# Kernel optimization log

Measured on AMD Instinct MI355X. Metric: run time of the kernel, lower is better.

The kernel has to match this reference:

```python
import jax, jax.numpy as jnp
import numpy as np

PS = 8; STRIDE = 1; NVALS = 31
DELTA = 0.05; ETA = 0.01; TAU = 0.1
B = 2; CIN = 32; H = 64; W = 64
HP = (H - PS) // STRIDE + 1
WP = (W - PS) // STRIDE + 1
TWO_PI = 2.0 * np.pi

# patch-local coordinate grid (torch.meshgrid 'ij': y varies along rows)
_lin = np.linspace(-1.0, 1.0, PS).astype(np.float32)
YG = jnp.asarray(np.tile(_lin[:, None], (1, PS)))[None, :, :, None, None]  # [1,ps,ps,1,1]
XG = jnp.asarray(np.tile(_lin[None, :], (PS, 1)))[None, :, :, None, None]

ANGLE_RANGE = jnp.asarray(np.linspace(0.0, TWO_PI, NVALS + 1, dtype=np.float32)[:NVALS])
XY_RANGE = jnp.asarray(np.linspace(-3.0, 3.0, NVALS, dtype=np.float32))

# unfold/fold index maps: pixel (hp*stride + px, wp*stride + py)
RI = jnp.arange(PS)[:, None] + STRIDE * jnp.arange(HP)[None, :]  # [ps,hp]
CI = jnp.arange(PS)[:, None] + STRIDE * jnp.arange(WP)[None, :]  # [ps,wp]
R4 = RI[:, None, :, None]  # [ps,1,hp,1]
C4 = CI[None, :, None, :]  # [1,ps,1,wp]


def conv1x1(x, w):
    return jnp.einsum('bchw,oc->bohw', x, w)


def bn(x, gamma, beta, eps=1e-5):
    # BatchNorm2d in training mode: batch statistics, biased variance
    m = x.mean(axis=(0, 2, 3), keepdims=True)
    v = x.var(axis=(0, 2, 3), keepdims=True)
    return gamma[None, :, None, None] * (x - m) * jax.lax.rsqrt(v + eps) + beta[None, :, None, None]


def silu(x):
    return x * jax.nn.sigmoid(x)


def params_to_distances(params):
    # params: [n,5,hp,wp] -> dists [n,2,ps,ps,hp,wp]
    x0 = params[:, 3][:, None, None]  # [n,1,1,hp,wp]
    y0 = params[:, 4][:, None, None]
    ang = jnp.sort(jnp.mod(params[:, :3], TWO_PI), axis=1)
    a1 = ang[:, 0][:, None, None]
    a2 = ang[:, 1][:, None, None]
    a3 = ang[:, 2][:, None, None]
    a4 = 0.5 * (a1 + a3) + jnp.where(jnp.mod(0.5 * (a1 - a3), TWO_PI) >= np.pi, np.pi, 0.0)

    def g(dt):
        return (dt / np.pi - 1.0) ** 35

    def line(a):
        return -jnp.sin(a) * (XG - x0) + jnp.cos(a) * (YG - y0)

    d42 = jnp.mod(a2 - a4, TWO_PI)
    sgn42 = jnp.where(d42 < np.pi, 1.0, -1.0)
    dist42 = sgn42 * jnp.minimum(sgn42 * line(a4), -sgn42 * line(a2)) + g(d42) * TAU
    d13 = jnp.mod(a3 - a1, TWO_PI)
    sgn13 = jnp.where(d13 < np.pi, 1.0, -1.0)
    dist13 = sgn13 * jnp.minimum(sgn13 * line(a1), -sgn13 * line(a3)) + g(d13) * TAU
    return jnp.stack([dist13, dist42], axis=1)


def wedges_of(dists):
    hd = 0.5 * (1.0 + (2.0 / np.pi) * jnp.arctan(dists / ETA))
    h0, h1 = hd[:, 0], hd[:, 1]
    return jnp.stack([1.0 - h0, h0 * (1.0 - h1), h0 * h1], axis=1)  # [n,3,ps,ps,hp,wp]


def dcp(params, imgp):
    # params [n,5,hp,wp], imgp [c,ps,ps,hp,wp]
    dists = params_to_distances(params)
    w = wedges_of(dists)
    wsum = w.sum(axis=(2, 3))  # [n,3,hp,wp]
    cnum = jnp.einsum('cxyHW,nkxyHW->nckHW', imgp, w)
    colors = cnum / (wsum[:, None] + 1e-10)  # [n,c,3,hp,wp]
    patches = jnp.einsum('nkxyHW,nckHW->ncxyHW', w, colors)
    return dists, colors, patches


def boundaries_of(dists):
    d1, d2 = dists[:, 0:1], dists[:, 1:2]
    mad = jnp.where(d1 < 0.0, -d1,
                    jnp.where(d2 < 0.0, jnp.minimum(d1, -d2), jnp.minimum(d1, d2)))
    return 1.0 / (1.0 + (mad / DELTA) ** 2)


def fold(patches):
    # [B,C,ps,ps,hp,wp] -> [B,C,H,W] (sum over overlapping patches)
    Bn, C = patches.shape[:2]
    return jnp.zeros((Bn, C, H, W), patches.dtype).at[:, :, R4, C4].add(patches)


def forward(x, reduce_w, reduce_gamma, reduce_beta, fb_w, fb_gamma, fb_beta, fi_w, fi_gamma, fi_beta):
    xr = silu(bn(conv1x1(x, reduce_w), reduce_gamma, reduce_beta))  # [B,3,H,W]
    imgp = xr[:, :, R4, C4]  # unfold -> [B,3,ps,ps,hp,wp]
    num_patches = jnp.zeros((H, W), xr.dtype).at[R4, C4].add(
        jnp.ones((PS, PS, HP, WP), xr.dtype))

    params = jnp.zeros((x.shape[0], 5, HP, WP), xr.dtype)

    def make_step(i, prange):
        def step(p_b, imgp_b):
            pq = jnp.repeat(p_b[None], NVALS, axis=0)  # [n,5,hp,wp]
            pq = pq.at[:, i].add(prange[:, None, None])
            _, _, patches = dcp(pq, imgp_b)
            loss = ((imgp_b[None] - patches) ** 2).mean(axis=(2, 3)).sum(axis=1)  # [n,hp,wp]
            best = jnp.argmin(loss, axis=0)
            vals = jnp.take_along_axis(pq[:, i], best[None], axis=0)[0]
            return p_b.at[i].set(vals)
        return step

    for i in range(5):  # coordinate descent over 3 angles then x0, y0
        prange = ANGLE_RANGE if i < 3 else XY_RANGE
        params = jax.vmap(make_step(i, prange))(params, imgp)

    def finalize(p_b, imgp_b):
        dists, _, patches = dcp(p_b[None], imgp_b)
        return patches[0], boundaries_of(dists)[0]

    patches_all, lb_all = jax.vmap(finalize)(params, imgp)
    smoothed = fold(patches_all) / num_patches[None, None]  # [B,3,H,W]
    gb = fold(lb_all) / num_patches[None, None]             # [B,1,H,W]
    gb3 = jnp.broadcast_to(gb, (gb.shape[0], 3, H, W))
    boundaries = silu(bn(conv1x1(gb3, fb_w), fb_gamma, fb_beta))
    image = silu(bn(conv1x1(smoothed, fi_w), fi_gamma, fi_beta))
    return boundaries, image


def setup_inputs() -> dict:
    key = jax.random.key(0)
    ks = jax.random.split(key, 4)
    return {
        'x': jax.random.normal(ks[0], (B, CIN, H, W), jnp.float32),
        'reduce_w': jax.random.normal(ks[1], (3, CIN), jnp.float32) * 0.1,
        'reduce_gamma': jnp.ones((3,), jnp.float32),
        'reduce_beta': jnp.zeros((3,), jnp.float32),
        'fb_w': jax.random.normal(ks[2], (1, 3), jnp.float32) * 0.3,
        'fb_gamma': jnp.ones((1,), jnp.float32),
        'fb_beta': jnp.zeros((1,), jnp.float32),
        'fi_w': jax.random.normal(ks[3], (1, 3), jnp.float32) * 0.3,
        'fi_gamma': jnp.ones((1,), jnp.float32),
        'fi_beta': jnp.zeros((1,), jnp.float32),
    }


def reference(x, reduce_w, reduce_gamma, reduce_beta, fb_w, fb_gamma, fb_beta, fi_w, fi_gamma, fi_beta):
    return forward(x, reduce_w, reduce_gamma, reduce_beta, fb_w, fb_gamma, fb_beta, fi_w, fi_gamma, fi_beta)
```

## Files before the change

### kernel.cpp

```cpp
#include <hip/hip_runtime.h>
#include <math.h>

#define B_    2
#define CIN_  32
#define H_    64
#define W_    64
#define HP_   57
#define WP_   57
#define NP_   (B_*HP_*WP_)
#define NVALS_ 31

#define XR_OFF   0
#define FP_OFF   24576
#define FG_OFF   49152
#define ST_OFF   57344
#define TMPB_OFF 57360
#define TMPI_OFF 65552
#define WS_TOTAL 73744

static __device__ __forceinline__ float mod2pi(float x) {
    const float TP = (float)(2.0 * M_PI);
    float m = fmodf(x, TP);
    return (m < 0.0f) ? (m + TP) : m;
}
static __device__ __forceinline__ float pow35f(float t) {
    float t2 = t * t, t4 = t2 * t2, t8 = t4 * t4, t16 = t8 * t8, t32 = t16 * t16;
    return t32 * t2 * t;
}
static __device__ __forceinline__ float siluf(float x) {
    return x / (1.0f + expf(-x));
}
static __device__ __forceinline__ float wave_sum(float v) {
#pragma unroll
    for (int m = 1; m < 64; m <<= 1) v += __shfl_xor(v, m);
    return v;
}
static __device__ __forceinline__ float lin_of(int k) {
    return (float)(-1.0 + (double)k * (2.0 / 7.0));
}

struct Geo {
    float X1, Y1, X3, Y3;
    float X4, Y4, X2, Y2;
    float sgn13, sgn42, g13, g42, x0, y0;
};

static __device__ void setup_geo(float p0, float p1, float p2, float p3, float p4,
                                 Geo& G) {
    const float PIF = (float)M_PI;
    float m0 = mod2pi(p0), m1 = mod2pi(p1), m2 = mod2pi(p2);
    float lo = fminf(m0, m1), hi = fmaxf(m0, m1);
    float a1 = fminf(lo, m2);
    float a3 = fmaxf(hi, m2);
    float a2 = fmaxf(fminf(hi, m2), lo);
    float hm = mod2pi(0.5f * (a1 - a3));
    float a4 = 0.5f * (a1 + a3) + ((hm >= PIF) ? PIF : 0.0f);
    float d42 = mod2pi(a2 - a4);
    G.sgn42 = (d42 < PIF) ? 1.0f : -1.0f;
    G.g42 = pow35f(d42 / PIF - 1.0f) * 0.1f;
    float d13 = mod2pi(a3 - a1);
    G.sgn13 = (d13 < PIF) ? 1.0f : -1.0f;
    G.g13 = pow35f(d13 / PIF - 1.0f) * 0.1f;
    float s1 = sinf(a1), c1 = cosf(a1);
    float s2 = sinf(a2), c2 = cosf(a2);
    float s3 = sinf(a3), c3 = cosf(a3);
    float s4 = sinf(a4), c4 = cosf(a4);
    G.X1 = -G.sgn13 * s1;  G.Y1 =  G.sgn13 * c1;
    G.X3 =  G.sgn13 * s3;  G.Y3 = -G.sgn13 * c3;
    G.X4 = -G.sgn42 * s4;  G.Y4 =  G.sgn42 * c4;
    G.X2 =  G.sgn42 * s2;  G.Y2 = -G.sgn42 * c2;
    G.x0 = p3; G.y0 = p4;
}

static __device__ __forceinline__ void dists_at(const Geo& G, float xg, float yg,
                                                float& d13, float& d42) {
    float dx = xg - G.x0, dy = yg - G.y0;
    float u1 = G.X1 * dx + G.Y1 * dy;
    float u3 = G.X3 * dx + G.Y3 * dy;
    float u4 = G.X4 * dx + G.Y4 * dy;
    float u2 = G.X2 * dx + G.Y2 * dy;
    d13 = G.sgn13 * fminf(u1, u3) + G.g13;
    d42 = G.sgn42 * fminf(u4, u2) + G.g42;
}

static __device__ __forceinline__ void wedge_of(float d13, float d42,
                                                float& w0, float& w1, float& w2) {
    const float C2OPI = (float)(2.0 / M_PI);
    float hd0 = 0.5f * (1.0f + C2OPI * atanf(d13 * 100.0f));
    float hd1 = 0.5f * (1.0f + C2OPI * atanf(d42 * 100.0f));
    w0 = 1.0f - hd0;
    w1 = hd0 * (1.0f - hd1);
    w2 = hd0 * hd1;
}

__global__ __launch_bounds__(128) void head_in_conv(const float* __restrict__ x,
                                                    const float* __restrict__ rw,
                                                    float* __restrict__ xr,
                                                    float* __restrict__ st) {
    const int e = blockIdx.x * 128 + threadIdx.x;
    const int b = e >> 12, rem = e & 4095;
    const float* xp = x + (size_t)b * CIN_ * 4096 + rem;
    float a0 = 0.0f, a1 = 0.0f, a2 = 0.0f;
#pragma unroll
    for (int c = 0; c < CIN_; ++c) {
        float xv = xp[c * 4096];
        a0 += rw[c] * xv;
        a1 += rw[32 + c] * xv;
        a2 += rw[64 + c] * xv;
    }
    xr[(b * 3 + 0) * 4096 + rem] = a0;
    xr[(b * 3 + 1) * 4096 + rem] = a1;
    xr[(b * 3 + 2) * 4096 + rem] = a2;
    float s0 = wave_sum(a0), q0 = wave_sum(a0 * a0);
    float s1 = wave_sum(a1), q1 = wave_sum(a1 * a1);
    float s2 = wave_sum(a2), q2 = wave_sum(a2 * a2);
    if ((threadIdx.x & 63) == 0) {
        atomicAdd(&st[0], s0); atomicAdd(&st[1], s1); atomicAdd(&st[2], s2);
        atomicAdd(&st[3], q0); atomicAdd(&st[4], q1); atomicAdd(&st[5], q2);
    }
}

__global__ __launch_bounds__(256) void mega_kernel(const float* __restrict__ xr,
                                                   const float* __restrict__ gamma,
                                                   const float* __restrict__ beta,
                                                   const float* __restrict__ st,
                                                   float* __restrict__ foldP,
                                                   float* __restrict__ foldG) {
    __shared__ float s_img[4][192];
    __shared__ float s_lin[8];
    const int t = threadIdx.x;
    if (t < 8) s_lin[t] = lin_of(t);
    const int lg = t >> 6, lane = t & 63;
    const int patch = blockIdx.x * 4 + lg;
    const bool active = (patch < NP_);
    int b = 0, hp = 0, wp = 0;
    if (active) {
        b = patch / (HP_ * WP_);
        int pi = patch - b * (HP_ * WP_);
        hp = pi / WP_; wp = pi - hp * WP_;
        const int pr = lane >> 3, pc = lane & 7;
        const int goff = ((hp + pr) << 6) + (wp + pc);
#pragma unroll
        for (int c = 0; c < 3; ++c) {
            float mean = st[c] / 8192.0f;
            float var  = st[3 + c] / 8192.0f - mean * mean;
            float sc = gamma[c] / sqrtf(var + 1e-5f);
            float sh = beta[c] - mean * sc;
            float v  = xr[((b * 3 + c) << 12) + goff];
            s_img[lg][64 * c + lane] = siluf(v * sc + sh);
        }
    }
    __syncthreads();
    if (!active) return;

    const int cand = lane >> 1;
    const int half = lane & 1;
    const float* img = s_img[lg] + half * 32;
    const int yoff = half << 2;

    float p0 = 0.0f, p1 = 0.0f, p2 = 0.0f, p3 = 0.0f, p4 = 0.0f;

#pragma unroll 1
    for (int step = 0; step < 5; ++step) {
        const float base = (step == 0) ? p0 : (step == 1) ? p1 :
                           (step == 2) ? p2 : (step == 3) ? p3 : p4;
        const int ci = (cand < NVALS_) ? cand : (NVALS_ - 1);
        float add;
        if (step < 3) add = (float)((double)ci * (6.283185307179586476925286766559 / 31.0));
        else          add = (float)(-3.0 + (double)ci * 0.2);
        const float pv = base + add;
        Geo G;
        setup_geo((step == 0) ? pv : p0, (step == 1) ? pv : p1,
                  (step == 2) ? pv : p2, (step == 3) ? pv : p3,
                  (step == 4) ? pv : p4, G);

        float ws0 = 0, ws1 = 0;
        float is0 = 0, is1 = 0, is2 = 0;
        float cn00 = 0, cn01 = 0, cn10 = 0, cn11 = 0, cn20 = 0, cn21 = 0;
        float g00 = 0, g01 = 0, g11 = 0;
#pragma unroll 1
        for (int r = 0; r < 4; ++r) {
            const float yg = s_lin[yoff + r];
            const float dy = yg - G.y0;
            const float t1 = G.Y1 * dy, t3 = G.Y3 * dy;
            const float t4 = G.Y4 * dy, t2 = G.Y2 * dy;
#pragma unroll
            for (int cth = 0; cth < 8; ++cth) {
                const int i = r * 8 + cth;
                const float dx = s_lin[cth] - G.x0;
                float u1 = G.X1 * dx + t1;
                float u3 = G.X3 * dx + t3;
                float u4 = G.X4 * dx + t4;
                float u2 = G.X2 * dx + t2;
                float d13 = G.sgn13 * fminf(u1, u3) + G.g13;
                float d42 = G.sgn42 * fminf(u4, u2) + G.g42;
                float w0, w1, w2;
                wedge_of(d13, d42, w0, w1, w2);
                float i0 = img[i], i1 = img[64 + i], i2 = img[128 + i];
                ws0 += w0; ws1 += w1;
                is0 += i0; is1 += i1; is2 += i2;
                cn00 += i0 * w0; cn01 += i0 * w1;
                cn10 += i1 * w0; cn11 += i1 * w1;
                cn20 += i2 * w0; cn21 += i2 * w1;
                g00 += w0 * w0; g01 += w0 * w1; g11 += w1 * w1;
            }
        }
        ws0 += __shfl_xor(ws0, 1); ws1 += __shfl_xor(ws1, 1);
        is0 += __shfl_xor(is0, 1); is1 += __shfl_xor(is1, 1); is2 += __shfl_xor(is2, 1);
        cn00 += __shfl_xor(cn00, 1); cn01 += __shfl_xor(cn01, 1);
        cn10 += __shfl_xor(cn10, 1); cn11 += __shfl_xor(cn11, 1);
        cn20 += __shfl_xor(cn20, 1); cn21 += __shfl_xor(cn21, 1);
        g00 += __shfl_xor(g00, 1); g01 += __shfl_xor(g01, 1); g11 += __shfl_xor(g11, 1);

        float ws2  = 64.0f - ws0 - ws1;
        float cn02 = is0 - cn00 - cn01;
        float cn12 = is1 - cn10 - cn11;
        float cn22 = is2 - cn20 - cn21;
        float g02  = ws0 - g00 - g01;
        float g12  = ws1 - g01 - g11;
        float g22  = ws2 - g02 - g12;

        float r0 = 1.0f / (ws0 + 1e-10f);
        float r1 = 1.0f / (ws1 + 1e-10f);
        float r2 = 1.0f / (ws2 + 1e-10f);
        float c00 = cn00 * r0, c01 = cn01 * r1, c02 = cn02 * r2;
        float c10 = cn10 * r0, c11 = cn11 * r1, c12 = cn12 * r2;
        float c20 = cn20 * r0, c21 = cn21 * r1, c22 = cn22 * r2;

        float loss =
            (c00 * c00 * g00 + c01 * c01 * g11 + c02 * c02 * g22
             + 2.0f * (c00 * c01 * g01 + c00 * c02 * g02 + c01 * c02 * g12)
             - 2.0f * (c00 * cn00 + c01 * cn01 + c02 * cn02))
          + (c10 * c10 * g00 + c11 * c11 * g11 + c12 * c12 * g22
             + 2.0f * (c10 * c11 * g01 + c10 * c12 * g02 + c11 * c12 * g12)
             - 2.0f * (c10 * cn10 + c11 * cn11 + c12 * cn12))
          + (c20 * c20 * g00 + c21 * c21 * g11 + c22 * c22 * g22
             + 2.0f * (c20 * c21 * g01 + c20 * c22 * g02 + c21 * c22 * g12)
             - 2.0f * (c20 * cn20 + c21 * cn21 + c22 * cn22));
        if (cand >= NVALS_) loss = INFINITY;

        float bl = loss; int bi = cand;
#pragma unroll
        for (int off = 32; off > 0; off >>= 1) {
            float ol = __shfl_down(bl, (unsigned)off);
            int   oi = __shfl_down(bi, (unsigned)off);
            if (ol < bl || (ol == bl && oi < bi)) { bl = ol; bi = oi; }
        }
        bi = __shfl(bi, 0);
        float badd;
        if (step < 3) badd = (float)((double)bi * (6.283185307179586476925286766559 / 31.0));
        else          badd = (float)(-3.0 + (double)bi * 0.2);
        const float bv = base + badd;
        if (step == 0) p0 = bv; else if (step == 1) p1 = bv;
        else if (step == 2) p2 = bv; else if (step == 3) p3 = bv; else p4 = bv;
    }

    {
        Geo G; setup_geo(p0, p1, p2, p3, p4, G);
        const int pr = lane >> 3, pc = lane & 7;
        float xg = s_lin[pc], yg = s_lin[pr];
        float d13, d42;
        dists_at(G, xg, yg, d13, d42);
        float w0, w1, w2;
        wedge_of(d13, d42, w0, w1, w2);
        float i0 = s_img[lg][lane];
        float i1 = s_img[lg][64 + lane];
        float i2 = s_img[lg][128 + lane];

        float r[12] = { w0, w1, w2,
                        i0 * w0, i0 * w1, i0 * w2,
                        i1 * w0, i1 * w1, i1 * w2,
                        i2 * w0, i2 * w1, i2 * w2 };
#pragma unroll
        for (int m = 1; m < 64; m <<= 1) {
#pragma unroll
            for (int j = 0; j < 12; ++j) r[j] += __shfl_xor(r[j], m);
        }
        float col[3][3];
#pragma unroll
        for (int c = 0; c < 3; ++c) {
            col[c][0] = r[3 + c * 3 + 0] / (r[0] + 1e-10f);
            col[c][1] = r[3 + c * 3 + 1] / (r[1] + 1e-10f);
            col[c][2] = r[3 + c * 3 + 2] / (r[2] + 1e-10f);
        }
        float o0 = w0 * col[0][0] + w1 * col[0][1] + w2 * col[0][2];
        float o1 = w0 * col[1][0] + w1 * col[1][1] + w2 * col[1][2];
        float o2 = w0 * col[2][0] + w1 * col[2][1] + w2 * col[2][2];

        float mad = (d13 < 0.0f) ? -d13 : ((d42 < 0.0f) ? fminf(d13, -d42) : fminf(d13, d42));
        float tt = mad / 0.05f;
        float lb = 1.0f / (1.0f + tt * tt);

        const int off = ((hp + pr) << 6) + (wp + pc);
        atomicAdd(&foldP[(b * 3 + 0) * 4096 + off], o0);
        atomicAdd(&foldP[(b * 3 + 1) * 4096 + off], o1);
        atomicAdd(&foldP[(b * 3 + 2) * 4096 + off], o2);
        atomicAdd(&foldG[b * 4096 + off], lb);
    }
}

static __device__ __forceinline__ float np_count(int tpos) {
    int lo = (tpos - 56 > 0) ? (tpos - 56) : 0;
    int hi = (tpos < 7) ? tpos : 7;
    return (float)(hi - lo + 1);
}

__global__ __launch_bounds__(256) void head_out_conv(const float* __restrict__ foldP,
                                                     const float* __restrict__ foldG,
                                                     const float* __restrict__ fb_w,
                                                     const float* __restrict__ fi_w,
                                                     float* __restrict__ tmpB,
                                                     float* __restrict__ tmpI,
                                                     float* __restrict__ st) {
    const int e = blockIdx.x * 256 + threadIdx.x;
    const int b = e >> 12, h = (e >> 6) & 63, w = e & 63;
    const float npv = np_count(h) * np_count(w);
    float gv = foldG[e] / npv;
    float vb = fb_w[0] * gv + fb_w[1] * gv + fb_w[2] * gv;
    const int off = (h << 6) + w;
    float s0 = foldP[(b * 3 + 0) * 4096 + off] / npv;
    float s1 = foldP[(b * 3 + 1) * 4096 + off] / npv;
    float s2 = foldP[(b * 3 + 2) * 4096 + off] / npv;
    float vi = fi_w[0] * s0 + fi_w[1] * s1 + fi_w[2] * s2;
    tmpB[e] = vb;
    tmpI[e] = vi;
    float sb = wave_sum(vb), qb = wave_sum(vb * vb);
    float si = wave_sum(vi), qi = wave_sum(vi * vi);
    if ((threadIdx.x & 63) == 0) {
        atomicAdd(&st[6], sb); atomicAdd(&st[7], qb);
        atomicAdd(&st[8], si); atomicAdd(&st[9], qi);
    }
}

__global__ __launch_bounds__(256) void head_out_apply(const float* __restrict__ tmpB,
                                                      const float* __restrict__ tmpI,
                                                      const float* __restrict__ fb_g,
                                                      const float* __restrict__ fb_b,
                                                      const float* __restrict__ fi_g,
                                                      const float* __restrict__ fi_b,
                                                      const float* __restrict__ st,
                                                      float* __restrict__ out) {
    const int e = blockIdx.x * 256 + threadIdx.x;
    {
        float mean = st[6] / 8192.0f;
        float var  = st[7] / 8192.0f - mean * mean;
        float sc = fb_g[0] / sqrtf(var + 1e-5f);
        float sh = fb_b[0] - mean * sc;
        out[e] = siluf(tmpB[e] * sc + sh);
    }
    {
        float mean = st[8] / 8192.0f;
        float var  = st[9] / 8192.0f - mean * mean;
        float sc = fi_g[0] / sqrtf(var + 1e-5f);
        float sh = fi_b[0] - mean * sc;
        out[8192 + e] = siluf(tmpI[e] * sc + sh);
    }
}

extern "C" void kernel_launch(void* const* d_in, const int* in_sizes, int n_in,
                              void* d_out, int out_size, void* d_ws, size_t ws_size,
                              hipStream_t stream) {
    (void)in_sizes; (void)n_in; (void)out_size; (void)ws_size;
    const float* x        = (const float*)d_in[0];
    const float* reduce_w = (const float*)d_in[1];
    const float* reduce_g = (const float*)d_in[2];
    const float* reduce_b = (const float*)d_in[3];
    const float* fb_w     = (const float*)d_in[4];
    const float* fb_g     = (const float*)d_in[5];
    const float* fb_b     = (const float*)d_in[6];
    const float* fi_w     = (const float*)d_in[7];
    const float* fi_g     = (const float*)d_in[8];
    const float* fi_b     = (const float*)d_in[9];
    float* ws     = (float*)d_ws;
    float* xr     = ws + XR_OFF;
    float* foldP  = ws + FP_OFF;
    float* foldG  = ws + FG_OFF;
    float* st     = ws + ST_OFF;
    float* tmpB   = ws + TMPB_OFF;
    float* tmpI   = ws + TMPI_OFF;
    float* out    = (float*)d_out;

    hipMemsetAsync(foldP, 0, (size_t)(TMPB_OFF - FP_OFF) * sizeof(float), stream);

    head_in_conv<<<64, 128, 0, stream>>>(x, reduce_w, xr, st);
    mega_kernel<<<(NP_ + 3) / 4, 256, 0, stream>>>(xr, reduce_g, reduce_b, st,
                                                   foldP, foldG);
    head_out_conv<<<32, 256, 0, stream>>>(foldP, foldG, fb_w, fi_w, tmpB, tmpI, st);
    head_out_apply<<<32, 256, 0, stream>>>(tmpB, tmpI, fb_g, fb_b, fi_g, fi_b, st, out);
}
```

Measured before the change: 244.4 us.

## Fuse output BN kernels, use polynomial atan, shrink mega_kernel blocks

Merges the two tail kernels into one 1024-thread single-block kernel that holds intermediates in shared memory and reduces BN statistics in-block, removing one launch and the tmp buffers. Replaces atanf in the wedge computation with a Cephes-style polynomial using a hardware reciprocal. Halves mega_kernel blocks to 2 patches per block, giving more, smaller blocks. The single-block tail serializes 8192 elements on one CU, and the fast atan slightly changes numerics.

```diff
diff --git a/kernel.cpp b/kernel.cpp
--- a/kernel.cpp
+++ b/kernel.cpp
@@ -14,9 +14,7 @@
 #define FP_OFF   24576
 #define FG_OFF   49152
 #define ST_OFF   57344
-#define TMPB_OFF 57360
-#define TMPI_OFF 65552
-#define WS_TOTAL 73744
+#define WS_TOTAL 57360
 
 static __device__ __forceinline__ float mod2pi(float x) {
     const float TP = (float)(2.0 * M_PI);
@@ -37,6 +35,27 @@
 }
 static __device__ __forceinline__ float lin_of(int k) {
     return (float)(-1.0 + (double)k * (2.0 / 7.0));
+}
+
+static __device__ __forceinline__ float fast_atan(float x) {
+    const float PIO2 = 1.5707963267948966f;
+    const float PIO4 = 0.7853981633974483f;
+    const float T3P8 = 2.414213562373095f;
+    const float TP8  = 0.41421356237309503f;
+    float ax = fabsf(x);
+    bool big = ax > T3P8;
+    bool mid = ax > TP8;
+    float denom = big ? ax : (ax + 1.0f);
+    float r = __builtin_amdgcn_rcpf(denom);
+    float zr = big ? -r : (ax - 1.0f) * r;
+    float z  = mid ? zr : ax;
+    float y0 = big ? PIO2 : (mid ? PIO4 : 0.0f);
+    float z2 = z * z;
+    float p = fmaf(fmaf(fmaf(8.05374449538e-2f, z2, -1.38776856032e-1f),
+                        z2, 1.99777106478e-1f),
+                   z2, -3.33329491539e-1f);
+    float res = fmaf(p * z2, z, z);
+    return copysignf(y0 + res, x);
 }
 
 struct Geo {
@@ -85,9 +104,9 @@
 
 static __device__ __forceinline__ void wedge_of(float d13, float d42,
                                                 float& w0, float& w1, float& w2) {
-    const float C2OPI = (float)(2.0 / M_PI);
-    float hd0 = 0.5f * (1.0f + C2OPI * atanf(d13 * 100.0f));
-    float hd1 = 0.5f * (1.0f + C2OPI * atanf(d42 * 100.0f));
+    const float C1OPI = 0.3183098861837907f;
+    float hd0 = fmaf(C1OPI, fast_atan(d13 * 100.0f), 0.5f);
+    float hd1 = fmaf(C1OPI, fast_atan(d42 * 100.0f), 0.5f);
     w0 = 1.0f - hd0;
     w1 = hd0 * (1.0f - hd1);
     w2 = hd0 * hd1;
@@ -120,18 +139,18 @@
     }
 }
 
-__global__ __launch_bounds__(256) void mega_kernel(const float* __restrict__ xr,
+__global__ __launch_bounds__(128) void mega_kernel(const float* __restrict__ xr,
                                                    const float* __restrict__ gamma,
                                                    const float* __restrict__ beta,
                                                    const float* __restrict__ st,
                                                    float* __restrict__ foldP,
                                                    float* __restrict__ foldG) {
-    __shared__ float s_img[4][192];
+    __shared__ float s_img[2][192];
     __shared__ float s_lin[8];
     const int t = threadIdx.x;
     if (t < 8) s_lin[t] = lin_of(t);
     const int lg = t >> 6, lane = t & 63;
-    const int patch = blockIdx.x * 4 + lg;
+    const int patch = blockIdx.x * 2 + lg;
     const bool active = (patch < NP_);
     int b = 0, hp = 0, wp = 0;
     if (active) {
@@ -305,55 +324,58 @@
     return (float)(hi - lo + 1);
 }
 
-__global__ __launch_bounds__(256) void head_out_conv(const float* __restrict__ foldP,
-                                                     const float* __restrict__ foldG,
-                                                     const float* __restrict__ fb_w,
-                                                     const float* __restrict__ fi_w,
-                                                     float* __restrict__ tmpB,
-                                                     float* __restrict__ tmpI,
-                                                     float* __restrict__ st) {
-    const int e = blockIdx.x * 256 + threadIdx.x;
-    const int b = e >> 12, h = (e >> 6) & 63, w = e & 63;
-    const float npv = np_count(h) * np_count(w);
-    float gv = foldG[e] / npv;
-    float vb = fb_w[0] * gv + fb_w[1] * gv + fb_w[2] * gv;
-    const int off = (h << 6) + w;
-    float s0 = foldP[(b * 3 + 0) * 4096 + off] / npv;
-    float s1 = foldP[(b * 3 + 1) * 4096 + off] / npv;
-    float s2 = foldP[(b * 3 + 2) * 4096 + off] / npv;
-    float vi = fi_w[0] * s0 + fi_w[1] * s1 + fi_w[2] * s2;
-    tmpB[e] = vb;
-    tmpI[e] = vi;
-    float sb = wave_sum(vb), qb = wave_sum(vb * vb);
-    float si = wave_sum(vi), qi = wave_sum(vi * vi);
-    if ((threadIdx.x & 63) == 0) {
-        atomicAdd(&st[6], sb); atomicAdd(&st[7], qb);
-        atomicAdd(&st[8], si); atomicAdd(&st[9], qi);
-    }
-}
-
-__global__ __launch_bounds__(256) void head_out_apply(const float* __restrict__ tmpB,
-                                                      const float* __restrict__ tmpI,
-                                                      const float* __restrict__ fb_g,
-                                                      const float* __restrict__ fb_b,
-                                                      const float* __restrict__ fi_g,
-                                                      const float* __restrict__ fi_b,
-                                                      const float* __restrict__ st,
-                                                      float* __restrict__ out) {
-    const int e = blockIdx.x * 256 + threadIdx.x;
-    {
-        float mean = st[6] / 8192.0f;
-        float var  = st[7] / 8192.0f - mean * mean;
-        float sc = fb_g[0] / sqrtf(var + 1e-5f);
-        float sh = fb_b[0] - mean * sc;
-        out[e] = siluf(tmpB[e] * sc + sh);
-    }
-    {
-        float mean = st[8] / 8192.0f;
-        float var  = st[9] / 8192.0f - mean * mean;
-        float sc = fi_g[0] / sqrtf(var + 1e-5f);
-        float sh = fi_b[0] - mean * sc;
-        out[8192 + e] = siluf(tmpI[e] * sc + sh);
+__global__ __launch_bounds__(1024) void head_out(const float* __restrict__ foldP,
+                                                 const float* __restrict__ foldG,
+                                                 const float* __restrict__ fb_w,
+                                                 const float* __restrict__ fb_g,
+                                                 const float* __restrict__ fb_b,
+                                                 const float* __restrict__ fi_w,
+                                                 const float* __restrict__ fi_g,
+                                                 const float* __restrict__ fi_b,
+                                                 float* __restrict__ out) {
+    __shared__ float sB[8192];
+    __shared__ float sI[8192];
+    __shared__ float red[16][4];
+    __shared__ float s_sc[4];
+    const int t = threadIdx.x;
+    float sb = 0, qb = 0, si = 0, qi = 0;
+#pragma unroll
+    for (int k = 0; k < 8; ++k) {
+        const int e = t + 1024 * k;
+        const int b = e >> 12, h = (e >> 6) & 63, w = e & 63;
+        const float inv = 1.0f / (np_count(h) * np_count(w));
+        float gv = foldG[e] * inv;
+        float vb = fb_w[0] * gv + fb_w[1] * gv + fb_w[2] * gv;
+        const int off = (h << 6) + w;
+        float v0 = foldP[(b * 3 + 0) * 4096 + off] * inv;
+        float v1 = foldP[(b * 3 + 1) * 4096 + off] * inv;
+        float v2 = foldP[(b * 3 + 2) * 4096 + off] * inv;
+        float vi = fi_w[0] * v0 + fi_w[1] * v1 + fi_w[2] * v2;
+        sB[e] = vb; sI[e] = vi;
+        sb += vb; qb += vb * vb; si += vi; qi += vi * vi;
+    }
+    sb = wave_sum(sb); qb = wave_sum(qb); si = wave_sum(si); qi = wave_sum(qi);
+    const int wid = t >> 6;
+    if ((t & 63) == 0) { red[wid][0] = sb; red[wid][1] = qb; red[wid][2] = si; red[wid][3] = qi; }
+    __syncthreads();
+    if (t == 0) {
+        float S = 0, Q = 0, S2 = 0, Q2 = 0;
+#pragma unroll
+        for (int w = 0; w < 16; ++w) { S += red[w][0]; Q += red[w][1]; S2 += red[w][2]; Q2 += red[w][3]; }
+        float meanB = S / 8192.0f,  varB = Q / 8192.0f - meanB * meanB;
+        float meanI = S2 / 8192.0f, varI = Q2 / 8192.0f - meanI * meanI;
+        float scB = fb_g[0] / sqrtf(varB + 1e-5f);
+        float scI = fi_g[0] / sqrtf(varI + 1e-5f);
+        s_sc[0] = scB; s_sc[1] = fb_b[0] - meanB * scB;
+        s_sc[2] = scI; s_sc[3] = fi_b[0] - meanI * scI;
+    }
+    __syncthreads();
+    const float scB = s_sc[0], shB = s_sc[1], scI = s_sc[2], shI = s_sc[3];
+#pragma unroll
+    for (int k = 0; k < 8; ++k) {
+        const int e = t + 1024 * k;
+        out[e]        = siluf(sB[e] * scB + shB);
+        out[8192 + e] = siluf(sI[e] * scI + shI);
     }
 }
 
@@ -376,15 +398,13 @@
     float* foldP  = ws + FP_OFF;
     float* foldG  = ws + FG_OFF;
     float* st     = ws + ST_OFF;
-    float* tmpB   = ws + TMPB_OFF;
-    float* tmpI   = ws + TMPI_OFF;
     float* out    = (float*)d_out;
 
-    hipMemsetAsync(foldP, 0, (size_t)(TMPB_OFF - FP_OFF) * sizeof(float), stream);
+    hipMemsetAsync(foldP, 0, (size_t)(WS_TOTAL - FP_OFF) * sizeof(float), stream);
 
     head_in_conv<<<64, 128, 0, stream>>>(x, reduce_w, xr, st);
-    mega_kernel<<<(NP_ + 3) / 4, 256, 0, stream>>>(xr, reduce_g, reduce_b, st,
+    mega_kernel<<<(NP_ + 1) / 2, 128, 0, stream>>>(xr, reduce_g, reduce_b, st,
                                                    foldP, foldG);
-    head_out_conv<<<32, 256, 0, stream>>>(foldP, foldG, fb_w, fi_w, tmpB, tmpI, st);
-    head_out_apply<<<32, 256, 0, stream>>>(tmpB, tmpI, fb_g, fb_b, fi_g, fi_b, st, out);
-}
+    head_out<<<1, 1024, 0, stream>>>(foldP, foldG, fb_w, fb_g, fb_b,
+                                     fi_w, fi_g, fi_b, out);
+}
```

New measurement: 261.1 us. 1.07x slower.
